# Performance work log

Measured on AMD Instinct MI355X. Metric: run time of the kernel, lower is better.

## Reference

```python
import jax, jax.numpy as jnp
import numpy as np

B, NLEV, NX, NXM = 1024, 60, 15, 12
NXS, NXS_RNN, NTOA = 24, 19, 2
NH1, NH2, NMEM, NY, NYS = 192, 192, 16, 5, 2


def _lstm(xg, h0, c0, Whh):
    # xg: [B,T,4H] precomputed input-to-gate projections (+bias); PyTorch gate order i,f,g,o
    def step(carry, xt):
        h, c = carry
        g = xt + h @ Whh.T
        i, f, gg, o = jnp.split(g, 4, axis=-1)
        c = jax.nn.sigmoid(f) * c + jax.nn.sigmoid(i) * jnp.tanh(gg)
        h = jax.nn.sigmoid(o) * jnp.tanh(c)
        return (h, c), h
    (hT, _), ys = jax.lax.scan(step, (h0, c0), jnp.swapaxes(xg, 0, 1))
    return jnp.swapaxes(ys, 0, 1), hT


def setup_inputs() -> dict:
    key = jax.random.key(0)
    ks = jax.random.split(key, 24)
    u = lambda k, s: jax.random.uniform(k, s, jnp.float32, 0.5, 1.5)
    n = lambda k, s, sc=0.05: jax.random.normal(k, s, jnp.float32) * sc
    NX1 = NXM + NMEM  # rnn1 input dim = 28
    return {
        'x_lev': n(ks[0], (B, NLEV, NX), 1.0),
        'x_sfc': n(ks[1], (B, NXS), 1.0),
        'memory': n(ks[2], (B, NLEV, NMEM), 1.0),
        'xmean_lev': n(ks[3], (NLEV, NX), 0.1),
        'xdiv_lev': u(ks[4], (NLEV, NX)),
        'xmean_sca': n(ks[5], (NXS,), 0.1),
        'xdiv_sca': u(ks[6], (NXS,)),
        'yscale_lev': u(ks[7], (NLEV, NY)),
        'yscale_sca': u(ks[8], (NYS,)),
        'W_sfc1': n(ks[9], (NH1, NXS_RNN)), 'b_sfc1': n(ks[9], (NH1,)),
        'W_sfc2': n(ks[10], (NH1, NXS_RNN)), 'b_sfc2': n(ks[10], (NH1,)),
        'W_toa1': n(ks[11], (NH2, NTOA)), 'b_toa1': n(ks[11], (NH2,)),
        'W_toa2': n(ks[12], (NH2, NTOA)), 'b_toa2': n(ks[12], (NH2,)),
        'W_ih1': n(ks[13], (4 * NH1, NX1)), 'W_hh1': n(ks[14], (4 * NH1, NH1)), 'b_1': n(ks[15], (4 * NH1,)),
        'W_ih2': n(ks[16], (4 * NH2, NH1)), 'W_hh2': n(ks[17], (4 * NH2, NH2)), 'b_2': n(ks[18], (4 * NH2,)),
        'W_lat': n(ks[19], (NMEM, NH2)), 'b_lat': n(ks[19], (NMEM,)),
        'W_out': n(ks[20], (NY, NMEM)), 'b_out': n(ks[20], (NY,)),
        'W_sfco': n(ks[21], (NYS, NH2)), 'b_sfco': n(ks[21], (NYS,)),
    }


def reference(x_lev, x_sfc, memory, xmean_lev, xdiv_lev, xmean_sca, xdiv_sca,
              yscale_lev, yscale_sca, W_sfc1, b_sfc1, W_sfc2, b_sfc2,
              W_toa1, b_toa1, W_toa2, b_toa2, W_ih1, W_hh1, b_1,
              W_ih2, W_hh2, b_2, W_lat, b_lat, W_out, b_out, W_sfco, b_sfco):
    # input normalization (buffers registered in __init__)
    x = (x_lev - xmean_lev) / xdiv_lev          # [B,L,15]
    xs = (x_sfc - xmean_sca) / xdiv_sca         # [B,24]
    # drop the 3 radiation-only level features (nx = nx - 3), append per-level memory
    x_main = jnp.concatenate([x[..., :NXM], memory], axis=-1)  # [B,L,28]
    xs_rnn = xs[:, :NXS_RNN]                    # surface features for rnn1 init
    x_toa = xs[:, :NTOA]                        # TOA (solar) features for rnn2 init
    # rnn1: bottom-up over levels (surface = last level index), init from surface MLPs
    h0 = jnp.tanh(xs_rnn @ W_sfc1.T + b_sfc1)
    c0 = jnp.tanh(xs_rnn @ W_sfc2.T + b_sfc2)
    xg1 = jnp.einsum('bli,gi->blg', jnp.flip(x_main, 1), W_ih1) + b_1  # [B,L,4H]
    y1, _ = _lstm(xg1, h0, c0, W_hh1)
    y1 = jnp.flip(y1, 1)                        # back to top-first order
    # rnn2: top-down, init from TOA MLPs
    h0b = jnp.tanh(x_toa @ W_toa1.T + b_toa1)
    c0b = jnp.tanh(x_toa @ W_toa2.T + b_toa2)
    xg2 = jnp.einsum('blh,gh->blg', y1, W_ih2) + b_2
    y2, h2_last = _lstm(xg2, h0b, c0b, W_hh2)
    # intermediate latent (nh_mem) then level outputs; postprocessing divides by yscale
    lat = y2 @ W_lat.T + b_lat                  # [B,L,16]
    out = (lat @ W_out.T + b_out) / yscale_lev  # [B,L,5]
    out_sfc = (h2_last @ W_sfco.T + b_sfco) / yscale_sca  # [B,2]
    return out, out_sfc
```

## Files before the change

kernel.cpp:

```cpp
#include <hip/hip_runtime.h>
#include <hip/hip_bf16.h>

using short8 = __attribute__((ext_vector_type(8))) short;
using f32x4  = __attribute__((ext_vector_type(4))) float;

#define B_     1024
#define NLEV_  60
#define NBLK_  64
#define ROWS_  16
#define QLEV_  15

__device__ __forceinline__ float bf2f(unsigned short u){
  unsigned int v = ((unsigned int)u) << 16;
  return __builtin_bit_cast(float, v);
}
__device__ __forceinline__ unsigned short f2bf(float x){
  __hip_bfloat16 h = __float2bfloat16(x);
  return __builtin_bit_cast(unsigned short, h);
}
__device__ __forceinline__ float sigm_(float x){
  return __builtin_amdgcn_rcpf(1.0f + __expf(-x));
}
__device__ __forceinline__ float tanh_(float x){
  return 1.0f - 2.0f*__builtin_amdgcn_rcpf(1.0f + __expf(2.0f*x));
}
__device__ __forceinline__ void softbar(){
  asm volatile("s_waitcnt lgkmcnt(0)" ::: "memory");
  __builtin_amdgcn_s_barrier();
  asm volatile("" ::: "memory");
}

__global__ void prep_weights_k(const float* __restrict__ Whh1, const float* __restrict__ Wih1,
                               const float* __restrict__ Whh2, const float* __restrict__ Wih2,
                               unsigned short* __restrict__ f_hh1, unsigned short* __restrict__ f_ih1,
                               unsigned short* __restrict__ f_hh2, unsigned short* __restrict__ f_ih2){
  int t = blockIdx.x*256 + threadIdx.x;
  if (t >= 912*64) return;
  int lane = t & 63;
  int fr   = t >> 6;
  int m    = lane & 15;
  int g16  = lane >> 4;
  short8 sv;
  unsigned short* dst;
  if (fr < 288){
    int nt = fr/6, kf = fr%6;
    int n = nt*16 + m, k0 = kf*32 + g16*8;
    #pragma unroll
    for (int j=0;j<8;j++) sv[j] = (short)f2bf(Whh1[n*192 + k0 + j]);
    dst = f_hh1 + (size_t)(fr*64 + lane)*8;
  } else if (fr < 336){
    int nt = fr - 288;
    int n = nt*16 + m, k0 = g16*8;
    #pragma unroll
    for (int j=0;j<8;j++){
      int k = k0 + j;
      sv[j] = (short)((k < 28) ? f2bf(Wih1[n*28 + k]) : (unsigned short)0);
    }
    dst = f_ih1 + (size_t)(nt*64 + lane)*8;
  } else if (fr < 624){
    int fl = fr - 336;
    int nt = fl/6, kf = fl%6;
    int n = nt*16 + m, k0 = kf*32 + g16*8;
    #pragma unroll
    for (int j=0;j<8;j++) sv[j] = (short)f2bf(Whh2[n*192 + k0 + j]);
    dst = f_hh2 + (size_t)(fl*64 + lane)*8;
  } else {
    int fl = fr - 624;
    int nt = fl/6, kf = fl%6;
    int n = nt*16 + m, k0 = kf*32 + g16*8;
    #pragma unroll
    for (int j=0;j<8;j++) sv[j] = (short)f2bf(Wih2[n*192 + k0 + j]);
    dst = f_ih2 + (size_t)(fl*64 + lane)*8;
  }
  *(short8*)dst = sv;
}

__global__ void wc_k(const float* __restrict__ W_lat, const float* __restrict__ b_lat,
                     const float* __restrict__ W_out, const float* __restrict__ b_out,
                     float* __restrict__ Wc, float* __restrict__ outb){
  int t = blockIdx.x*256 + threadIdx.x;
  if (t < 960){
    int n = t / 192, k = t % 192;
    float a = 0.f;
    #pragma unroll
    for (int j=0;j<16;j++) a += W_out[n*16+j] * W_lat[j*192+k];
    Wc[t] = a;
  } else if (t < 965){
    int n = t - 960;
    float a = b_out[n];
    #pragma unroll
    for (int j=0;j<16;j++) a += W_out[n*16+j] * b_lat[j];
    outb[n] = a;
  }
}

__global__ void prep_x_k(const float* __restrict__ x_lev, const float* __restrict__ xmean_lev,
                         const float* __restrict__ xdiv_lev, const float* __restrict__ memv,
                         unsigned short* __restrict__ xfrag){
  int t = blockIdx.x*256 + threadIdx.x;
  if (t >= NBLK_*NLEV_*64) return;
  int lane = t & 63;
  int lev  = (t >> 6) % NLEV_;
  int blk  = t / (NLEV_*64);
  int m    = lane & 15;
  int b    = blk*ROWS_ + m;
  int k0   = (lane >> 4)*8;
  short8 sv;
  #pragma unroll
  for (int j=0;j<8;j++){
    int k = k0 + j;
    float val = 0.0f;
    if (k < 12)      val = (x_lev[(size_t)(b*NLEV_+lev)*15 + k] - xmean_lev[lev*15+k]) / xdiv_lev[lev*15+k];
    else if (k < 28) val = memv[(size_t)(b*NLEV_+lev)*16 + (k-12)];
    sv[j] = (short)f2bf(val);
  }
  *(short8*)(xfrag + (size_t)((blk*NLEV_+lev)*64 + lane)*8) = sv;
}

__global__ void init_states_k(const float* __restrict__ x_sfc, const float* __restrict__ xmean_sca,
                              const float* __restrict__ xdiv_sca,
                              const float* __restrict__ Ws1, const float* __restrict__ bs1,
                              const float* __restrict__ Ws2, const float* __restrict__ bs2,
                              const float* __restrict__ Wt1, const float* __restrict__ bt1,
                              const float* __restrict__ Wt2, const float* __restrict__ bt2,
                              float* __restrict__ h0, float* __restrict__ c0,
                              float* __restrict__ h0b, float* __restrict__ c0b){
  int t = blockIdx.x*256 + threadIdx.x;
  if (t >= B_*192) return;
  int b = t / 192, n = t % 192;
  float a1 = bs1[n], a2 = bs2[n];
  for (int j=0;j<19;j++){
    float xs = (x_sfc[b*24+j] - xmean_sca[j]) / xdiv_sca[j];
    a1 += xs * Ws1[n*19+j];
    a2 += xs * Ws2[n*19+j];
  }
  h0[t] = tanh_(a1); c0[t] = tanh_(a2);
  float a3 = bt1[n], a4 = bt2[n];
  for (int j=0;j<2;j++){
    float xt = (x_sfc[b*24+j] - xmean_sca[j]) / xdiv_sca[j];
    a3 += xt * Wt1[n*2+j];
    a4 += xt * Wt2[n*2+j];
  }
  h0b[t] = tanh_(a3); c0b[t] = tanh_(a4);
}

__global__ __launch_bounds__(768)
__attribute__((amdgpu_waves_per_eu(3,3)))
void lstm1_k(
    const float* __restrict__ h0, const float* __restrict__ c0,
    const unsigned short* __restrict__ f_hh1, const unsigned short* __restrict__ f_ih1,
    const unsigned short* __restrict__ xfrag, const float* __restrict__ b1,
    unsigned short* __restrict__ y1frag){
  __shared__ alignas(16) unsigned short h_s[2][16][200];
  int tid = threadIdx.x;
  int w = tid >> 6, l = tid & 63;
  int blk = blockIdx.x, b0 = blk*ROWS_;
  int m = l & 15, g4 = l >> 4, m0 = g4*4;
  int col = w*16 + m;

  const short8* whh_p = (const short8*)f_hh1;
  const short8* wih_p = (const short8*)f_ih1;
  short8 whh[4][6], wih[4];
  #pragma unroll
  for (int g=0; g<4; g++){
    int nt = 12*g + w;
    wih[g] = wih_p[nt*64 + l];
    #pragma unroll
    for (int kf=0; kf<6; kf++) whh[g][kf] = whh_p[(nt*6 + kf)*64 + l];
  }
  float bias[4];
  #pragma unroll
  for (int g=0; g<4; g++) bias[g] = b1[g*192 + col];
  float c[4];
  #pragma unroll
  for (int r=0; r<4; r++){
    c[r] = c0[(size_t)(b0+m0+r)*192 + col];
    h_s[0][m0+r][col] = f2bf(h0[(size_t)(b0+m0+r)*192 + col]);
  }
  __syncthreads();

  const short8* xfp = (const short8*)xfrag + (size_t)blk*NLEV_*64;
  short8 ax = xfp[(NLEV_-1)*64 + l];
  for (int t=0; t<NLEV_; t++){
    int cur = t & 1;
    int lsrc = NLEV_-1 - t;
    short8 ax_n = xfp[(lsrc > 0 ? lsrc-1 : 0)*64 + l];
    f32x4 acc[4];
    #pragma unroll
    for (int g=0; g<4; g++){ acc[g][0]=bias[g]; acc[g][1]=bias[g]; acc[g][2]=bias[g]; acc[g][3]=bias[g]; }
    #pragma unroll
    for (int g=0; g<4; g++)
      acc[g] = __builtin_amdgcn_mfma_f32_16x16x32_bf16(ax, wih[g], acc[g], 0, 0, 0);
    #pragma unroll
    for (int kf=0; kf<6; kf++){
      short8 ah = *(const short8*)&h_s[cur][m][kf*32 + g4*8];
      #pragma unroll
      for (int g=0; g<4; g++)
        acc[g] = __builtin_amdgcn_mfma_f32_16x16x32_bf16(ah, whh[g][kf], acc[g], 0, 0, 0);
    }
    #pragma unroll
    for (int r=0; r<4; r++){
      float gi=acc[0][r], gf=acc[1][r], gg=acc[2][r], go=acc[3][r];
      float cn = sigm_(gf)*c[r] + sigm_(gi)*tanh_(gg);
      float hn = sigm_(go)*tanh_(cn);
      c[r] = cn;
      h_s[cur^1][m0+r][col] = f2bf(hn);
    }
    softbar();
    if (w < 6){
      short8 v = *(const short8*)&h_s[cur^1][m][w*32 + g4*8];
      *(short8*)(y1frag + ((size_t)(blk*NLEV_+lsrc)*6 + w)*512 + (size_t)l*8) = v;
    }
    ax = ax_n;
  }
}

__global__ __launch_bounds__(768)
__attribute__((amdgpu_waves_per_eu(3,3)))
void xg_gemm_k(
    const unsigned short* __restrict__ y1frag, const unsigned short* __restrict__ f_ih2,
    const float* __restrict__ b2, float* __restrict__ xgq, int lev0){
  int tid = threadIdx.x;
  int w = tid >> 6, l = tid & 63;
  int blk = blockIdx.x / 5, lg = blockIdx.x % 5;
  const short8* yfp   = (const short8*)y1frag;
  const short8* wih_p = (const short8*)f_ih2;
  f32x4 acc[3][4];
  #pragma unroll
  for (int g=0; g<4; g++){
    float bv = b2[g*192 + 16*w + (l&15)];
    #pragma unroll
    for (int j=0; j<3; j++){ acc[j][g][0]=bv; acc[j][g][1]=bv; acc[j][g][2]=bv; acc[j][g][3]=bv; }
  }
  #pragma unroll
  for (int kf=0; kf<6; kf++){
    short8 wb[4];
    #pragma unroll
    for (int g=0; g<4; g++) wb[g] = wih_p[((12*g + w)*6 + kf)*64 + l];
    #pragma unroll
    for (int j=0; j<3; j++){
      short8 ay = yfp[((size_t)(blk*NLEV_ + lev0 + lg*3 + j)*6 + kf)*64 + l];
      #pragma unroll
      for (int g=0; g<4; g++)
        acc[j][g] = __builtin_amdgcn_mfma_f32_16x16x32_bf16(ay, wb[g], acc[j][g], 0, 0, 0);
    }
  }
  #pragma unroll
  for (int j=0; j<3; j++){
    int tl = lg*3 + j;
    #pragma unroll
    for (int g=0; g<4; g++)
      *(f32x4*)&xgq[(((size_t)blk*QLEV_ + tl)*48 + 12*g + w)*256 + (size_t)l*4] = acc[j][g];
  }
}

__global__ __launch_bounds__(768)
__attribute__((amdgpu_waves_per_eu(3,3)))
void lstm2r_k(
    const float* __restrict__ hin, const float* __restrict__ cin,
    const unsigned short* __restrict__ f_hh2, const float* __restrict__ xgq,
    unsigned short* __restrict__ y2, float* __restrict__ h2T,
    float* __restrict__ hcar, float* __restrict__ ccar,
    int t0, int last){
  __shared__ alignas(16) unsigned short h_s[2][16][200];
  int tid = threadIdx.x;
  int w = tid >> 6, l = tid & 63;
  int blk = blockIdx.x, b0 = blk*ROWS_;
  int m = l & 15, g4 = l >> 4, m0 = g4*4;
  int col = w*16 + m;
  int row_ = (w*64 + l)/24, cg_ = (w*64 + l)%24;

  const short8* whh_p = (const short8*)f_hh2;
  short8 whh[4][6];
  #pragma unroll
  for (int g=0; g<4; g++){
    int nt = 12*g + w;
    #pragma unroll
    for (int kf=0; kf<6; kf++) whh[g][kf] = whh_p[(nt*6 + kf)*64 + l];
  }
  float c[4];
  #pragma unroll
  for (int r=0; r<4; r++){
    c[r] = cin[(size_t)(b0+m0+r)*192 + col];
    h_s[0][m0+r][col] = f2bf(hin[(size_t)(b0+m0+r)*192 + col]);
  }
  __syncthreads();

  const f32x4* xp = (const f32x4*)xgq + (size_t)blk*QLEV_*48*64;
  f32x4 xg[4], xgn[4];
  #pragma unroll
  for (int g=0; g<4; g++) xg[g] = xp[(size_t)(12*g + w)*64 + l];

  for (int tl=0; tl<QLEV_; tl++){
    int cur = tl & 1;
    int tln = (tl < QLEV_-1) ? tl+1 : tl;
    #pragma unroll
    for (int g=0; g<4; g++) xgn[g] = xp[((size_t)tln*48 + 12*g + w)*64 + l];

    f32x4 acc[4];
    #pragma unroll
    for (int g=0; g<4; g++) acc[g] = xg[g];
    #pragma unroll
    for (int kf=0; kf<6; kf++){
      short8 ah = *(const short8*)&h_s[cur][m][kf*32 + g4*8];
      #pragma unroll
      for (int g=0; g<4; g++)
        acc[g] = __builtin_amdgcn_mfma_f32_16x16x32_bf16(ah, whh[g][kf], acc[g], 0, 0, 0);
    }
    float hf[4];
    #pragma unroll
    for (int r=0; r<4; r++){
      float gi=acc[0][r], gf=acc[1][r], gg=acc[2][r], go=acc[3][r];
      float cn = sigm_(gf)*c[r] + sigm_(gi)*tanh_(gg);
      float hn = sigm_(go)*tanh_(cn);
      c[r] = cn;
      hf[r] = hn;
      h_s[cur^1][m0+r][col] = f2bf(hn);
    }
    if (tl == QLEV_-1){
      #pragma unroll
      for (int r=0; r<4; r++){
        hcar[(size_t)(b0+m0+r)*192 + col] = hf[r];
        ccar[(size_t)(b0+m0+r)*192 + col] = c[r];
      }
      if (last){
        #pragma unroll
        for (int r=0; r<4; r++) h2T[(size_t)(b0+m0+r)*192 + col] = hf[r];
      }
    }
    softbar();
    if (w < 6){
      int t = t0 + tl;
      short8 v = *(const short8*)&h_s[cur^1][row_][cg_*8];
      *(short8*)(y2 + ((size_t)(b0+row_)*NLEV_ + t)*192 + cg_*8) = v;
    }
    #pragma unroll
    for (int g=0; g<4; g++) xg[g] = xgn[g];
  }
}

__global__ void heads_k(const unsigned short* __restrict__ y2, const float* __restrict__ Wc,
                        const float* __restrict__ outb, const float* __restrict__ yscale_lev,
                        float* __restrict__ out){
  __shared__ alignas(16) unsigned short yl[48][200];
  int tid = threadIdx.x;
  int row0 = blockIdx.x*48;
  for (int ci = tid; ci < 48*24; ci += 256){
    int r = ci/24, cgi = ci%24;
    short8 v = *(const short8*)(y2 + ((size_t)(row0+r))*192 + cgi*8);
    *(short8*)&yl[r][cgi*8] = v;
  }
  __syncthreads();
  if (tid < 240){
    int r = tid/5, n = tid - 5*r;
    int row = row0 + r;
    float acc = outb[n];
    const float* wc = Wc + n*192;
    #pragma unroll
    for (int cgi=0; cgi<24; cgi++){
      short8 y8 = *(const short8*)&yl[r][cgi*8];
      #pragma unroll
      for (int j=0;j<8;j++) acc += bf2f((unsigned short)y8[j]) * wc[cgi*8+j];
    }
    int lev = row % NLEV_;
    out[(size_t)row*5 + n] = acc / yscale_lev[lev*5 + n];
  }
}

__global__ void sfc_k(const float* __restrict__ h2T, const float* __restrict__ W_sfco,
                      const float* __restrict__ b_sfco, const float* __restrict__ yscale_sca,
                      float* __restrict__ out_sfc){
  int t = blockIdx.x*256 + threadIdx.x;
  if (t >= B_*2) return;
  int b = t >> 1, j = t & 1;
  float acc = b_sfco[j];
  for (int k=0;k<192;k++) acc += h2T[(size_t)b*192+k] * W_sfco[j*192+k];
  out_sfc[t] = acc / yscale_sca[j];
}

extern "C" void kernel_launch(void* const* d_in, const int* in_sizes, int n_in,
                              void* d_out, int out_size, void* d_ws, size_t ws_size,
                              hipStream_t stream){
  const float* x_lev     = (const float*)d_in[0];
  const float* x_sfc     = (const float*)d_in[1];
  const float* memory_   = (const float*)d_in[2];
  const float* xmean_lev = (const float*)d_in[3];
  const float* xdiv_lev  = (const float*)d_in[4];
  const float* xmean_sca = (const float*)d_in[5];
  const float* xdiv_sca  = (const float*)d_in[6];
  const float* yscale_lev= (const float*)d_in[7];
  const float* yscale_sca= (const float*)d_in[8];
  const float* W_sfc1    = (const float*)d_in[9];
  const float* b_sfc1    = (const float*)d_in[10];
  const float* W_sfc2    = (const float*)d_in[11];
  const float* b_sfc2    = (const float*)d_in[12];
  const float* W_toa1    = (const float*)d_in[13];
  const float* b_toa1    = (const float*)d_in[14];
  const float* W_toa2    = (const float*)d_in[15];
  const float* b_toa2    = (const float*)d_in[16];
  const float* W_ih1     = (const float*)d_in[17];
  const float* W_hh1     = (const float*)d_in[18];
  const float* b_1       = (const float*)d_in[19];
  const float* W_ih2     = (const float*)d_in[20];
  const float* W_hh2     = (const float*)d_in[21];
  const float* b_2       = (const float*)d_in[22];
  const float* W_lat     = (const float*)d_in[23];
  const float* b_lat     = (const float*)d_in[24];
  const float* W_out     = (const float*)d_in[25];
  const float* b_out     = (const float*)d_in[26];
  const float* W_sfco    = (const float*)d_in[27];
  const float* b_sfco    = (const float*)d_in[28];

  char* ws = (char*)d_ws;
  float* h0            = (float*)(ws + 0);
  float* c0            = (float*)(ws + 786432);
  float* h0b           = (float*)(ws + 1572864);
  float* c0b           = (float*)(ws + 2359296);
  unsigned short* f_hh1= (unsigned short*)(ws + 3145728);
  unsigned short* f_ih1= (unsigned short*)(ws + 3440640);
  unsigned short* f_hh2= (unsigned short*)(ws + 3489792);
  unsigned short* f_ih2= (unsigned short*)(ws + 3784704);
  unsigned short* xfrag= (unsigned short*)(ws + 4079616);
  unsigned short* y1frag=(unsigned short*)(ws + 8011776);
  unsigned short* y2   = (unsigned short*)(ws + 31604736);
  float* h2T           = (float*)(ws + 55197696);
  float* Wc            = (float*)(ws + 55984128);
  float* outb          = (float*)(ws + 55987968);
  float* hcar          = (float*)(ws + 55988224);
  float* ccar          = (float*)(ws + 56774656);
  float* xgq           = (float*)(ws + 57561088);

  float* out    = (float*)d_out;
  float* outsfc = out + (size_t)B_*NLEV_*5;

  prep_weights_k<<<228, 256, 0, stream>>>(W_hh1, W_ih1, W_hh2, W_ih2, f_hh1, f_ih1, f_hh2, f_ih2);
  wc_k<<<4, 256, 0, stream>>>(W_lat, b_lat, W_out, b_out, Wc, outb);
  prep_x_k<<<960, 256, 0, stream>>>(x_lev, xmean_lev, xdiv_lev, memory_, xfrag);
  init_states_k<<<768, 256, 0, stream>>>(x_sfc, xmean_sca, xdiv_sca,
                                         W_sfc1, b_sfc1, W_sfc2, b_sfc2,
                                         W_toa1, b_toa1, W_toa2, b_toa2,
                                         h0, c0, h0b, c0b);
  lstm1_k<<<NBLK_, 768, 0, stream>>>(h0, c0, f_hh1, f_ih1, xfrag, b_1, y1frag);
  for (int q = 0; q < 4; q++){
    xg_gemm_k<<<320, 768, 0, stream>>>(y1frag, f_ih2, b_2, xgq, q*QLEV_);
    lstm2r_k<<<NBLK_, 768, 0, stream>>>(q == 0 ? h0b : hcar, q == 0 ? c0b : ccar,
                                        f_hh2, xgq, y2, h2T, hcar, ccar,
                                        q*QLEV_, q == 3 ? 1 : 0);
  }
  heads_k<<<1280, 256, 0, stream>>>(y2, Wc, outb, yscale_lev, out);
  sfc_k<<<8, 256, 0, stream>>>(h2T, W_sfco, b_sfco, yscale_sca, outsfc);
}
```

Measured before the change: 339.2 us.

## Stream recurrent LSTM weights through triple-buffered LDS via async global_load_lds

Instead of holding all recurrent weight fragments in registers, both LSTM kernels repack the weights so each K-chunk is contiguous. They then stream the chunks from global memory into a three-slot LDS ring with global_load_lds, synchronising with a barrier per chunk. The per-step output store is deferred to the next step, which removes the extra barrier after each step. This frees registers and drops the waves_per_eu constraint, but it re-reads weights from L2 every timestep and adds several barriers per step on a latency-bound recurrence.

```diff
diff --git a/kernel.cpp b/kernel.cpp
--- a/kernel.cpp
+++ b/kernel.cpp
@@ -2,6 +2,7 @@
 #include <hip/hip_bf16.h>
 
 using short8 = __attribute__((ext_vector_type(8))) short;
+using s4_    = __attribute__((ext_vector_type(4))) short;
 using f32x4  = __attribute__((ext_vector_type(4))) float;
 
 #define B_     1024
@@ -10,6 +11,9 @@
 #define ROWS_  16
 #define QLEV_  15
 
+#define AS1(p) ((const __attribute__((address_space(1))) void*)(p))
+#define AS3(p) ((__attribute__((address_space(3))) void*)(p))
+
 __device__ __forceinline__ float bf2f(unsigned short u){
   unsigned int v = ((unsigned int)u) << 16;
   return __builtin_bit_cast(float, v);
@@ -32,8 +36,8 @@
 
 __global__ void prep_weights_k(const float* __restrict__ Whh1, const float* __restrict__ Wih1,
                                const float* __restrict__ Whh2, const float* __restrict__ Wih2,
-                               unsigned short* __restrict__ f_hh1, unsigned short* __restrict__ f_ih1,
-                               unsigned short* __restrict__ f_hh2, unsigned short* __restrict__ f_ih2){
+                               unsigned short* __restrict__ f_all1, unsigned short* __restrict__ f_all2,
+                               unsigned short* __restrict__ f_ih2){
   int t = blockIdx.x*256 + threadIdx.x;
   if (t >= 912*64) return;
   int lane = t & 63;
@@ -42,28 +46,29 @@
   int g16  = lane >> 4;
   short8 sv;
   unsigned short* dst;
-  if (fr < 288){
-    int nt = fr/6, kf = fr%6;
-    int n = nt*16 + m, k0 = kf*32 + g16*8;
-    #pragma unroll
-    for (int j=0;j<8;j++) sv[j] = (short)f2bf(Whh1[n*192 + k0 + j]);
-    dst = f_hh1 + (size_t)(fr*64 + lane)*8;
-  } else if (fr < 336){
-    int nt = fr - 288;
+  if (fr < 48){
+    int nt = fr;
     int n = nt*16 + m, k0 = g16*8;
     #pragma unroll
     for (int j=0;j<8;j++){
       int k = k0 + j;
       sv[j] = (short)((k < 28) ? f2bf(Wih1[n*28 + k]) : (unsigned short)0);
     }
-    dst = f_ih1 + (size_t)(nt*64 + lane)*8;
+    dst = f_all1 + ((size_t)(0*48 + nt)*64 + lane)*8;
+  } else if (fr < 336){
+    int q = fr - 48;
+    int kf = q/48, nt = q%48;
+    int n = nt*16 + m, k0 = kf*32 + g16*8;
+    #pragma unroll
+    for (int j=0;j<8;j++) sv[j] = (short)f2bf(Whh1[n*192 + k0 + j]);
+    dst = f_all1 + ((size_t)((1+kf)*48 + nt)*64 + lane)*8;
   } else if (fr < 624){
-    int fl = fr - 336;
-    int nt = fl/6, kf = fl%6;
+    int q = fr - 336;
+    int kf = q/48, nt = q%48;
     int n = nt*16 + m, k0 = kf*32 + g16*8;
     #pragma unroll
     for (int j=0;j<8;j++) sv[j] = (short)f2bf(Whh2[n*192 + k0 + j]);
-    dst = f_hh2 + (size_t)(fl*64 + lane)*8;
+    dst = f_all2 + ((size_t)(kf*48 + nt)*64 + lane)*8;
   } else {
     int fl = fr - 624;
     int nt = fl/6, kf = fl%6;
@@ -144,30 +149,33 @@
   h0b[t] = tanh_(a3); c0b[t] = tanh_(a4);
 }
 
-__global__ __launch_bounds__(768)
-__attribute__((amdgpu_waves_per_eu(3,3)))
-void lstm1_k(
+__global__ __launch_bounds__(768, 1) void lstm1_k(
     const float* __restrict__ h0, const float* __restrict__ c0,
-    const unsigned short* __restrict__ f_hh1, const unsigned short* __restrict__ f_ih1,
+    const unsigned short* __restrict__ f_all1,
     const unsigned short* __restrict__ xfrag, const float* __restrict__ b1,
     unsigned short* __restrict__ y1frag){
   __shared__ alignas(16) unsigned short h_s[2][16][200];
+  __shared__ alignas(16) unsigned short wbuf[3][48*512];
   int tid = threadIdx.x;
   int w = tid >> 6, l = tid & 63;
   int blk = blockIdx.x, b0 = blk*ROWS_;
   int m = l & 15, g4 = l >> 4, m0 = g4*4;
   int col = w*16 + m;
-
-  const short8* whh_p = (const short8*)f_hh1;
-  const short8* wih_p = (const short8*)f_ih1;
-  short8 whh[4][6], wih[4];
-  #pragma unroll
-  for (int g=0; g<4; g++){
-    int nt = 12*g + w;
-    wih[g] = wih_p[nt*64 + l];
-    #pragma unroll
-    for (int kf=0; kf<6; kf++) whh[g][kf] = whh_p[(nt*6 + kf)*64 + l];
-  }
+  int sq  = tid*4;
+  int skf = sq >> 9, srem = sq & 511;
+  int sli = srem >> 3, sj0 = srem & 7;
+  int shrow = sli & 15, shcol = skf*32 + (sli>>4)*8 + sj0;
+
+  auto issue1 = [&](int gidx){
+    int src = gidx % 7;
+    int buf = gidx % 3;
+    const unsigned short* g = f_all1 + (size_t)src*48*512 + (size_t)(w*4)*512 + (size_t)l*8;
+    unsigned short* lp = &wbuf[buf][(w*4)*512];
+    #pragma unroll
+    for (int r=0; r<4; r++)
+      __builtin_amdgcn_global_load_lds(AS1(g + r*512), AS3(lp + r*512), 16, 0, 0);
+  };
+
   float bias[4];
   #pragma unroll
   for (int g=0; g<4; g++) bias[g] = b1[g*192 + col];
@@ -177,26 +185,46 @@
     c[r] = c0[(size_t)(b0+m0+r)*192 + col];
     h_s[0][m0+r][col] = f2bf(h0[(size_t)(b0+m0+r)*192 + col]);
   }
-  __syncthreads();
-
   const short8* xfp = (const short8*)xfrag + (size_t)blk*NLEV_*64;
   short8 ax = xfp[(NLEV_-1)*64 + l];
+  issue1(0);
+  issue1(1);
+  __syncthreads();
+
+  int gc = 0;
   for (int t=0; t<NLEV_; t++){
     int cur = t & 1;
     int lsrc = NLEV_-1 - t;
-    short8 ax_n = xfp[(lsrc > 0 ? lsrc-1 : 0)*64 + l];
+    short8 ax_n = ax;
     f32x4 acc[4];
     #pragma unroll
     for (int g=0; g<4; g++){ acc[g][0]=bias[g]; acc[g][1]=bias[g]; acc[g][2]=bias[g]; acc[g][3]=bias[g]; }
     #pragma unroll
-    for (int g=0; g<4; g++)
-      acc[g] = __builtin_amdgcn_mfma_f32_16x16x32_bf16(ax, wih[g], acc[g], 0, 0, 0);
-    #pragma unroll
-    for (int kf=0; kf<6; kf++){
-      short8 ah = *(const short8*)&h_s[cur][m][kf*32 + g4*8];
-      #pragma unroll
-      for (int g=0; g<4; g++)
-        acc[g] = __builtin_amdgcn_mfma_f32_16x16x32_bf16(ah, whh[g][kf], acc[g], 0, 0, 0);
+    for (int ch=0; ch<7; ch++){
+      if (ch == 2) asm volatile("s_waitcnt vmcnt(5) lgkmcnt(0)" ::: "memory");
+      else         asm volatile("s_waitcnt vmcnt(4) lgkmcnt(0)" ::: "memory");
+      __builtin_amdgcn_s_barrier();
+      asm volatile("" ::: "memory");
+      issue1(gc+2);
+      if (ch == 1){
+        ax_n = xfp[(lsrc > 0 ? lsrc-1 : 0)*64 + l];
+        int tprev = (t > 0) ? t-1 : 0;
+        int lstore = NLEV_-1 - tprev;
+        s4_ v = *(const s4_*)&h_s[t & 1][shrow][shcol];
+        *(s4_*)(y1frag + ((size_t)(blk*NLEV_+lstore)*6 + skf)*512 + (size_t)sli*8 + sj0) = v;
+      }
+      const short8* wb = (const short8*)&wbuf[gc%3][0];
+      if (ch == 0){
+        #pragma unroll
+        for (int g=0; g<4; g++)
+          acc[g] = __builtin_amdgcn_mfma_f32_16x16x32_bf16(ax, wb[(12*g + w)*64 + l], acc[g], 0, 0, 0);
+      } else {
+        short8 ah = *(const short8*)&h_s[cur][m][(ch-1)*32 + g4*8];
+        #pragma unroll
+        for (int g=0; g<4; g++)
+          acc[g] = __builtin_amdgcn_mfma_f32_16x16x32_bf16(ah, wb[(12*g + w)*64 + l], acc[g], 0, 0, 0);
+      }
+      gc++;
     }
     #pragma unroll
     for (int r=0; r<4; r++){
@@ -206,18 +234,16 @@
       c[r] = cn;
       h_s[cur^1][m0+r][col] = f2bf(hn);
     }
-    softbar();
-    if (w < 6){
-      short8 v = *(const short8*)&h_s[cur^1][m][w*32 + g4*8];
-      *(short8*)(y1frag + ((size_t)(blk*NLEV_+lsrc)*6 + w)*512 + (size_t)l*8) = v;
-    }
     ax = ax_n;
   }
-}
-
-__global__ __launch_bounds__(768)
-__attribute__((amdgpu_waves_per_eu(3,3)))
-void xg_gemm_k(
+  softbar();
+  {
+    s4_ v = *(const s4_*)&h_s[0][shrow][shcol];
+    *(s4_*)(y1frag + ((size_t)(blk*NLEV_))*6*512 + (size_t)skf*512 + (size_t)sli*8 + sj0) = v;
+  }
+}
+
+__global__ __launch_bounds__(768, 1) void xg_gemm_k(
     const unsigned short* __restrict__ y1frag, const unsigned short* __restrict__ f_ih2,
     const float* __restrict__ b2, float* __restrict__ xgq, int lev0){
   int tid = threadIdx.x;
@@ -254,58 +280,73 @@
   }
 }
 
-__global__ __launch_bounds__(768)
-__attribute__((amdgpu_waves_per_eu(3,3)))
-void lstm2r_k(
+__global__ __launch_bounds__(768, 1) void lstm2r_k(
     const float* __restrict__ hin, const float* __restrict__ cin,
-    const unsigned short* __restrict__ f_hh2, const float* __restrict__ xgq,
+    const unsigned short* __restrict__ f_all2, const float* __restrict__ xgq,
     unsigned short* __restrict__ y2, float* __restrict__ h2T,
     float* __restrict__ hcar, float* __restrict__ ccar,
     int t0, int last){
   __shared__ alignas(16) unsigned short h_s[2][16][200];
+  __shared__ alignas(16) unsigned short wbuf[3][48*512];
   int tid = threadIdx.x;
   int w = tid >> 6, l = tid & 63;
   int blk = blockIdx.x, b0 = blk*ROWS_;
   int m = l & 15, g4 = l >> 4, m0 = g4*4;
   int col = w*16 + m;
-  int row_ = (w*64 + l)/24, cg_ = (w*64 + l)%24;
-
-  const short8* whh_p = (const short8*)f_hh2;
-  short8 whh[4][6];
-  #pragma unroll
-  for (int g=0; g<4; g++){
-    int nt = 12*g + w;
-    #pragma unroll
-    for (int kf=0; kf<6; kf++) whh[g][kf] = whh_p[(nt*6 + kf)*64 + l];
-  }
+  int srow = tid / 48, scs = (tid % 48) * 4;
+
+  auto issue2 = [&](int gidx){
+    int src = gidx % 6;
+    int buf = gidx % 3;
+    const unsigned short* g = f_all2 + (size_t)src*48*512 + (size_t)(w*4)*512 + (size_t)l*8;
+    unsigned short* lp = &wbuf[buf][(w*4)*512];
+    #pragma unroll
+    for (int r=0; r<4; r++)
+      __builtin_amdgcn_global_load_lds(AS1(g + r*512), AS3(lp + r*512), 16, 0, 0);
+  };
+
   float c[4];
   #pragma unroll
   for (int r=0; r<4; r++){
     c[r] = cin[(size_t)(b0+m0+r)*192 + col];
     h_s[0][m0+r][col] = f2bf(hin[(size_t)(b0+m0+r)*192 + col]);
   }
-  __syncthreads();
-
   const f32x4* xp = (const f32x4*)xgq + (size_t)blk*QLEV_*48*64;
   f32x4 xg[4], xgn[4];
   #pragma unroll
   for (int g=0; g<4; g++) xg[g] = xp[(size_t)(12*g + w)*64 + l];
-
+  issue2(0);
+  issue2(1);
+  __syncthreads();
+
+  int gc = 0;
   for (int tl=0; tl<QLEV_; tl++){
     int cur = tl & 1;
-    int tln = (tl < QLEV_-1) ? tl+1 : tl;
-    #pragma unroll
-    for (int g=0; g<4; g++) xgn[g] = xp[((size_t)tln*48 + 12*g + w)*64 + l];
-
     f32x4 acc[4];
     #pragma unroll
     for (int g=0; g<4; g++) acc[g] = xg[g];
     #pragma unroll
-    for (int kf=0; kf<6; kf++){
-      short8 ah = *(const short8*)&h_s[cur][m][kf*32 + g4*8];
+    for (int ch=0; ch<6; ch++){
+      if (ch == 2) asm volatile("s_waitcnt vmcnt(8) lgkmcnt(0)" ::: "memory");
+      else         asm volatile("s_waitcnt vmcnt(4) lgkmcnt(0)" ::: "memory");
+      __builtin_amdgcn_s_barrier();
+      asm volatile("" ::: "memory");
+      issue2(gc+2);
+      if (ch == 1){
+        int tln = (tl < QLEV_-1) ? tl+1 : tl;
+        #pragma unroll
+        for (int g=0; g<4; g++) xgn[g] = xp[((size_t)tln*48 + 12*g + w)*64 + l];
+        int tprev = (tl > 0) ? tl-1 : 0;
+        int lev = t0 + tprev;
+        s4_ v = *(const s4_*)&h_s[tl & 1][srow][scs];
+        *(s4_*)(y2 + ((size_t)(b0+srow)*NLEV_ + lev)*192 + scs) = v;
+      }
+      const short8* wb = (const short8*)&wbuf[gc%3][0];
+      short8 ah = *(const short8*)&h_s[cur][m][ch*32 + g4*8];
       #pragma unroll
       for (int g=0; g<4; g++)
-        acc[g] = __builtin_amdgcn_mfma_f32_16x16x32_bf16(ah, whh[g][kf], acc[g], 0, 0, 0);
+        acc[g] = __builtin_amdgcn_mfma_f32_16x16x32_bf16(ah, wb[(12*g + w)*64 + l], acc[g], 0, 0, 0);
+      gc++;
     }
     float hf[4];
     #pragma unroll
@@ -328,14 +369,13 @@
         for (int r=0; r<4; r++) h2T[(size_t)(b0+m0+r)*192 + col] = hf[r];
       }
     }
-    softbar();
-    if (w < 6){
-      int t = t0 + tl;
-      short8 v = *(const short8*)&h_s[cur^1][row_][cg_*8];
-      *(short8*)(y2 + ((size_t)(b0+row_)*NLEV_ + t)*192 + cg_*8) = v;
-    }
     #pragma unroll
     for (int g=0; g<4; g++) xg[g] = xgn[g];
+  }
+  softbar();
+  {
+    s4_ v = *(const s4_*)&h_s[QLEV_ & 1][srow][scs];
+    *(s4_*)(y2 + ((size_t)(b0+srow)*NLEV_ + (t0 + QLEV_-1))*192 + scs) = v;
   }
 }
 
@@ -416,9 +456,8 @@
   float* c0            = (float*)(ws + 786432);
   float* h0b           = (float*)(ws + 1572864);
   float* c0b           = (float*)(ws + 2359296);
-  unsigned short* f_hh1= (unsigned short*)(ws + 3145728);
-  unsigned short* f_ih1= (unsigned short*)(ws + 3440640);
-  unsigned short* f_hh2= (unsigned short*)(ws + 3489792);
+  unsigned short* f_all1=(unsigned short*)(ws + 3145728);
+  unsigned short* f_all2=(unsigned short*)(ws + 3489792);
   unsigned short* f_ih2= (unsigned short*)(ws + 3784704);
   unsigned short* xfrag= (unsigned short*)(ws + 4079616);
   unsigned short* y1frag=(unsigned short*)(ws + 8011776);
@@ -433,18 +472,18 @@
   float* out    = (float*)d_out;
   float* outsfc = out + (size_t)B_*NLEV_*5;
 
-  prep_weights_k<<<228, 256, 0, stream>>>(W_hh1, W_ih1, W_hh2, W_ih2, f_hh1, f_ih1, f_hh2, f_ih2);
+  prep_weights_k<<<228, 256, 0, stream>>>(W_hh1, W_ih1, W_hh2, W_ih2, f_all1, f_all2, f_ih2);
   wc_k<<<4, 256, 0, stream>>>(W_lat, b_lat, W_out, b_out, Wc, outb);
   prep_x_k<<<960, 256, 0, stream>>>(x_lev, xmean_lev, xdiv_lev, memory_, xfrag);
   init_states_k<<<768, 256, 0, stream>>>(x_sfc, xmean_sca, xdiv_sca,
                                          W_sfc1, b_sfc1, W_sfc2, b_sfc2,
                                          W_toa1, b_toa1, W_toa2, b_toa2,
                                          h0, c0, h0b, c0b);
-  lstm1_k<<<NBLK_, 768, 0, stream>>>(h0, c0, f_hh1, f_ih1, xfrag, b_1, y1frag);
+  lstm1_k<<<NBLK_, 768, 0, stream>>>(h0, c0, f_all1, xfrag, b_1, y1frag);
   for (int q = 0; q < 4; q++){
     xg_gemm_k<<<320, 768, 0, stream>>>(y1frag, f_ih2, b_2, xgq, q*QLEV_);
     lstm2r_k<<<NBLK_, 768, 0, stream>>>(q == 0 ? h0b : hcar, q == 0 ? c0b : ccar,
-                                        f_hh2, xgq, y2, h2T, hcar, ccar,
+                                        f_all2, xgq, y2, h2T, hcar, ccar,
                                         q*QLEV_, q == 3 ? 1 : 0);
   }
   heads_k<<<1280, 256, 0, stream>>>(y2, Wc, outb, yscale_lev, out);
```

After: 630.8 us. 1.86x slower.
